# Performance work log

Hardware: AMD Instinct MI355X
Metric: run time of the kernel (lower is better)

The kernel has to match this reference:

```python
import jax, jax.numpy as jnp
import numpy as np

D_MODEL = 1024
NUM_HEADS = 16
HEAD_DIM = D_MODEL // NUM_HEADS


def setup_inputs() -> dict:
    key = jax.random.key(0)
    k0, k1, k2, k3, k4 = jax.random.split(key, 5)
    B, S, D = 4, 2048, D_MODEL
    std = np.sqrt(2.0 / (D + D)).astype(np.float32)
    return {
        "in_features": jax.random.normal(k0, (B, S, D), dtype=jnp.float32),
        "Wq": jax.random.normal(k1, (D, D), dtype=jnp.float32) * std,
        "Wk": jax.random.normal(k2, (D, D), dtype=jnp.float32) * std,
        "Wv": jax.random.normal(k3, (D, D), dtype=jnp.float32) * std,
        "Wo": jax.random.normal(k4, (D, D), dtype=jnp.float32) * std,
    }


def reference(in_features, Wq, Wk, Wv, Wo):
    B, S, D = in_features.shape
    H, Hd = NUM_HEADS, HEAD_DIM

    def split_heads(x):  # (B,S,D) -> (B,H,S,Hd)
        return x.reshape(B, S, H, Hd).transpose(0, 2, 1, 3)

    q = split_heads(in_features @ Wq.T)
    k = split_heads(in_features @ Wk.T)
    v = split_heads(in_features @ Wv.T)

    scale = 1.0 / jnp.sqrt(jnp.asarray(Hd, dtype=q.dtype))
    scores = jnp.einsum("bhsd,bhtd->bhst", q, k) * scale  # (B,H,S,S)
    causal = jnp.tril(jnp.ones((S, S), dtype=bool))  # (S,S)
    scores = jnp.where(causal[None, None], scores, -jnp.inf)
    attn = jax.nn.softmax(scores, axis=-1)
    out = jnp.einsum("bhst,bhtd->bhsd", attn, v)  # (B,H,S,Hd)
    out = out.transpose(0, 2, 1, 3).reshape(B, S, D)
    return out @ Wo.T
```

## Files before the change

kernel.cpp:

```cpp
#include <hip/hip_runtime.h>


typedef float f32x4 __attribute__((ext_vector_type(4)));
typedef float f32x16 __attribute__((ext_vector_type(16)));
typedef short s16x8 __attribute__((ext_vector_type(8)));

#if __has_builtin(__builtin_amdgcn_exp2f)
#define EXP2(x) __builtin_amdgcn_exp2f(x)
#else
#define EXP2(x) exp2f(x)
#endif

__device__ __forceinline__ unsigned short f2bf(float f) {
  unsigned int u = __float_as_uint(f);
  u += 0x7fffu + ((u >> 16) & 1u);
  return (unsigned short)(u >> 16);
}

__device__ __forceinline__ unsigned int pk2bf(float f0, float f1) {
  return __builtin_amdgcn_perm(__float_as_uint(f1) + 0x8000u,
                               __float_as_uint(f0) + 0x8000u, 0x07060302u);
}

__device__ __forceinline__ unsigned int pk2bf_t(float f0, float f1) {
  return __builtin_amdgcn_perm(__float_as_uint(f1), __float_as_uint(f0), 0x07060302u);
}

__device__ __forceinline__ void gl_lds16(const short* g, short* lds) {
  __builtin_amdgcn_global_load_lds(
      (const __attribute__((address_space(1))) unsigned int*)g,
      (__attribute__((address_space(3))) unsigned int*)lds, 16, 0, 0);
}

__global__ __launch_bounds__(256) void cvt_all(const float4* __restrict__ X,
                                               const float4* __restrict__ Wq,
                                               const float4* __restrict__ Wk,
                                               const float4* __restrict__ Wv,
                                               const float4* __restrict__ Wo,
                                               ushort4* __restrict__ xb,
                                               ushort4* __restrict__ wqkv,
                                               ushort4* __restrict__ wob) {
  const int NX = 8192 * 1024 / 4;
  const int NW = 1024 * 1024 / 4;
  const int NT = NX + 4 * NW;
  int i = blockIdx.x * blockDim.x + threadIdx.x;
  int stride = gridDim.x * blockDim.x;
  for (int idx = i; idx < NT; idx += stride) {
    const float4* s;
    ushort4* d;
    int off;
    if (idx < NX) {
      s = X; d = xb; off = idx;
    } else {
      int j = idx - NX;
      int w = j >> 18;
      off = j & (NW - 1);
      switch (w) {
        case 0: s = Wq; d = wqkv; break;
        case 1: s = Wk; d = wqkv + NW; break;
        case 2: s = Wv; d = wqkv + 2 * NW; break;
        default: s = Wo; d = wob; break;
      }
    }
    float4 f = s[off];
    ushort4 r;
    r.x = f2bf(f.x); r.y = f2bf(f.y); r.z = f2bf(f.z); r.w = f2bf(f.w);
    d[off] = r;
  }
}

template <int MODE>
__global__ __launch_bounds__(256) void gemm_bt(const short* __restrict__ A,
                                               const short* __restrict__ B,
                                               float* __restrict__ Cf,
                                               short* __restrict__ q_o,
                                               short* __restrict__ k_o,
                                               short* __restrict__ vT_o,
                                               int M, int N, int K) {
  const int tid = threadIdx.x;
  const int wave = tid >> 6, lane = tid & 63;
  const int quad = lane >> 4, l15 = lane & 15;
  const int m0 = blockIdx.x * 128, n0 = blockIdx.y * 128;
  const int wm = (wave >> 1) * 64, wn = (wave & 1) * 64;

  __shared__ __align__(16) short As[128 * 64];
  __shared__ __align__(16) short Bs[128 * 64];

  const f32x4 z4 = {0.f, 0.f, 0.f, 0.f};
  f32x4 acc[4][4];
  for (int i = 0; i < 4; ++i)
    for (int j = 0; j < 4; ++j) acc[i][j] = z4;

  for (int k0 = 0; k0 < K; k0 += 64) {
    __syncthreads();
    for (int i = 0; i < 4; ++i) {
      int c = wave * 4 + i;
      int r = c * 8 + (lane >> 3);
      int c8 = (lane & 7) ^ (r & 7);
      gl_lds16(A + (size_t)(m0 + r) * K + k0 + c8 * 8, As + c * 512 + lane * 8);
      gl_lds16(B + (size_t)(n0 + r) * K + k0 + c8 * 8, Bs + c * 512 + lane * 8);
    }
    __syncthreads();
    for (int kk = 0; kk < 64; kk += 32) {
      int c8b = (kk >> 3) + quad;
      s16x8 af[4], bfr[4];
      for (int mt = 0; mt < 4; ++mt) {
        int row = wm + mt * 16 + l15;
        af[mt] = *(const s16x8*)(As + row * 64 + ((c8b ^ (row & 7)) << 3));
      }
      for (int nt = 0; nt < 4; ++nt) {
        int row = wn + nt * 16 + l15;
        bfr[nt] = *(const s16x8*)(Bs + row * 64 + ((c8b ^ (row & 7)) << 3));
      }
      for (int mt = 0; mt < 4; ++mt)
        for (int nt = 0; nt < 4; ++nt)
          acc[mt][nt] = __builtin_amdgcn_mfma_f32_16x16x32_bf16(af[mt], bfr[nt],
                                                                acc[mt][nt], 0, 0, 0);
    }
  }

  if (MODE == 0) {
    for (int mt = 0; mt < 4; ++mt)
      for (int nt = 0; nt < 4; ++nt) {
        int col = n0 + wn + nt * 16 + l15;
        for (int r = 0; r < 4; ++r) {
          int row = m0 + wm + mt * 16 + quad * 4 + r;
          Cf[(size_t)row * N + col] = acc[mt][nt][r];
        }
      }
  } else {
    if (n0 < 1024) {
      const float scale = 0.18033688011112042f;
      for (int mt = 0; mt < 4; ++mt)
        for (int nt = 0; nt < 4; ++nt) {
          int col = n0 + wn + nt * 16 + l15;
          for (int r = 0; r < 4; ++r) {
            int row = m0 + wm + mt * 16 + quad * 4 + r;
            ((unsigned short*)q_o)[(size_t)row * 1024 + col] = f2bf(acc[mt][nt][r] * scale);
          }
        }
    } else if (n0 < 2048) {
      for (int mt = 0; mt < 4; ++mt)
        for (int nt = 0; nt < 4; ++nt) {
          int col = n0 - 1024 + wn + nt * 16 + l15;
          for (int r = 0; r < 4; ++r) {
            int row = m0 + wm + mt * 16 + quad * 4 + r;
            ((unsigned short*)k_o)[(size_t)row * 1024 + col] = f2bf(acc[mt][nt][r]);
          }
        }
    } else {
      for (int mt = 0; mt < 4; ++mt)
        for (int nt = 0; nt < 4; ++nt) {
          int col = n0 - 2048 + wn + nt * 16 + l15;
          int h = col >> 6, d = col & 63;
          int row0 = m0 + wm + mt * 16 + quad * 4;
          int b = row0 >> 11, s = row0 & 2047;
          uint2 pk;
          pk.x = pk2bf(acc[mt][nt][0], acc[mt][nt][1]);
          pk.y = pk2bf(acc[mt][nt][2], acc[mt][nt][3]);
          *(uint2*)((unsigned short*)vT_o + (((size_t)b * 16 + h) * 64 + d) * 2048 + s) = pk;
        }
    }
  }
}

__global__ __launch_bounds__(256, 2) void attn_kernel(const short* __restrict__ qb,
                                                      const short* __restrict__ kb,
                                                      const short* __restrict__ vT,
                                                      short* __restrict__ ob) {
  const int bh = blockIdx.x;
  const int qt = 15 - (int)blockIdx.y;
  const int tid = threadIdx.x;
  const int wave = tid >> 6, lane = tid & 63;
  const int l31 = lane & 31, h = lane >> 5;
  const int q0 = qt * 128;
  const size_t rowbase = (size_t)(bh >> 4) * 2048;
  const int hoff = (bh & 15) * 64;

  __shared__ __align__(16) short Ks[2][8192];
  __shared__ __align__(16) short VTs[2][8192];

  const int kc = wave * 4;
  const int kr = kc * 8 + (lane >> 3);
  const short* ksrc = kb + (rowbase + kr) * 1024 + hoff + (((lane & 7) ^ (kr & 7)) << 3);
  const int vg = lane & 15;
  const short* vsrc_i[4];
#pragma unroll
  for (int i = 0; i < 4; ++i) {
    int d = (kc + i) * 4 + (lane >> 4);
    vsrc_i[i] = vT + ((size_t)bh * 64 + d) * 2048 + ((vg ^ (d & 7)) << 3);
  }

  s16x8 qf[4];
  {
    const short* qrow = qb + (rowbase + q0 + wave * 32 + l31) * 1024 + hoff + h * 8;
#pragma unroll
    for (int k = 0; k < 4; ++k) qf[k] = *(const s16x8*)(qrow + k * 16);
  }

#pragma unroll
  for (int i = 0; i < 4; ++i)
    gl_lds16(ksrc + i * 8 * 1024, Ks[0] + (kc + i) * 512 + lane * 8);
#pragma unroll
  for (int i = 0; i < 4; ++i)
    gl_lds16(vsrc_i[i], VTs[0] + (kc + i) * 512 + lane * 8);

  f32x16 oacc[2];
#pragma unroll
  for (int dt = 0; dt < 2; ++dt)
#pragma unroll
    for (int e = 0; e < 16; ++e) oacc[dt][e] = 0.f;
  float lacc = 0.f;
  const int kswz = l31 & 7;

  for (int t = 0; t <= qt; ++t) {
    __syncthreads();
    const int cur = t & 1;

    if (t < qt) {
      const int nxt = cur ^ 1;
      const short* ks = ksrc + (size_t)(t + 1) * 128 * 1024;
#pragma unroll
      for (int i = 0; i < 4; ++i)
        gl_lds16(ks + i * 8 * 1024, Ks[nxt] + (kc + i) * 512 + lane * 8);
#pragma unroll
      for (int i = 0; i < 4; ++i)
        gl_lds16(vsrc_i[i] + (t + 1) * 128, VTs[nxt] + (kc + i) * 512 + lane * 8);
    }

    const short* Kc = Ks[cur];
    const short* Vc = VTs[cur];

    unsigned int pp[4][8];
    float sum = 0.f;
#pragma unroll
    for (int g = 0; g < 2; ++g) {
      f32x16 s0, s1;
#pragma unroll
      for (int e = 0; e < 16; ++e) { s0[e] = 0.f; s1[e] = 0.f; }
#pragma unroll
      for (int ks = 0; ks < 4; ++ks) {
        int pos = ((ks << 1) + h) ^ kswz;
        s16x8 kf0 = *(const s16x8*)(Kc + ((2 * g) * 32 + l31) * 64 + (pos << 3));
        s16x8 kf1 = *(const s16x8*)(Kc + ((2 * g + 1) * 32 + l31) * 64 + (pos << 3));
        s0 = __builtin_amdgcn_mfma_f32_32x32x16_bf16(kf0, qf[ks], s0, 0, 0, 0);
        s1 = __builtin_amdgcn_mfma_f32_32x32x16_bf16(kf1, qf[ks], s1, 0, 0, 0);
      }
      if (t == qt) {
        int qg = wave * 32 + l31;
#pragma unroll
        for (int e = 0; e < 16; ++e) {
          int rloc = (e & 3) + 8 * (e >> 2) + 4 * h;
          if ((2 * g) * 32 + rloc > qg) s0[e] = -1e30f;
          if ((2 * g + 1) * 32 + rloc > qg) s1[e] = -1e30f;
        }
      }
#pragma unroll
      for (int rg = 0; rg < 8; ++rg) {
        float a0 = EXP2(s0[2 * rg]), a1 = EXP2(s0[2 * rg + 1]);
        float b0 = EXP2(s1[2 * rg]), b1 = EXP2(s1[2 * rg + 1]);
        sum += (a0 + a1) + (b0 + b1);
        pp[2 * g][rg] = pk2bf_t(a0, a1);
        pp[2 * g + 1][rg] = pk2bf_t(b0, b1);
      }
    }
    lacc += sum;

#pragma unroll
    for (int s = 0; s < 8; ++s) {
      int m = s >> 1, base = (s & 1) * 4;
      unsigned int ax = pp[m][base + 0], ay = pp[m][base + 1];
      unsigned int bx = pp[m][base + 2], by = pp[m][base + 3];
      unsigned int sx = h ? ax : bx, sy = h ? ay : by;
      unsigned int rx = (unsigned int)__shfl_xor((int)sx, 32);
      unsigned int ry = (unsigned int)__shfl_xor((int)sy, 32);
      union { s16x8 v; unsigned int u[4]; } pf;
      pf.u[0] = h ? rx : ax;
      pf.u[1] = h ? ry : ay;
      pf.u[2] = h ? bx : rx;
      pf.u[3] = h ? by : ry;
#pragma unroll
      for (int dt = 0; dt < 2; ++dt) {
        int d = dt * 32 + l31;
        s16x8 vf = *(const s16x8*)(Vc + d * 128 + ((((s << 1) + h) ^ (d & 7)) << 3));
        oacc[dt] = __builtin_amdgcn_mfma_f32_32x32x16_bf16(vf, pf.v, oacc[dt], 0, 0, 0);
      }
    }
  }

  lacc += __shfl_xor(lacc, 32);
  float inv = 1.0f / lacc;
  size_t row = rowbase + q0 + wave * 32 + l31;
  unsigned short* orow = (unsigned short*)ob + row * 1024 + hoff;
#pragma unroll
  for (int dt = 0; dt < 2; ++dt)
#pragma unroll
    for (int rg = 0; rg < 4; ++rg) {
      int d = dt * 32 + rg * 8 + 4 * h;
      uint2 pk;
      pk.x = pk2bf(oacc[dt][rg * 4 + 0] * inv, oacc[dt][rg * 4 + 1] * inv);
      pk.y = pk2bf(oacc[dt][rg * 4 + 2] * inv, oacc[dt][rg * 4 + 3] * inv);
      *(uint2*)(orow + d) = pk;
    }
}

extern "C" void kernel_launch(void* const* d_in, const int* in_sizes, int n_in,
                              void* d_out, int out_size, void* d_ws, size_t ws_size,
                              hipStream_t stream) {
  const float* X  = (const float*)d_in[0];
  const float* Wq = (const float*)d_in[1];
  const float* Wk = (const float*)d_in[2];
  const float* Wv = (const float*)d_in[3];
  const float* Wo = (const float*)d_in[4];

  short* xb   = (short*)d_ws;
  short* wqkv = xb + (size_t)8192 * 1024;
  short* wob  = wqkv + (size_t)3072 * 1024;
  short* qb   = wob + (size_t)1024 * 1024;
  short* kb   = qb + (size_t)8192 * 1024;
  short* vT   = kb + (size_t)8192 * 1024;
  short* ob   = xb;

  const int MB = 8192;

  cvt_all<<<3072, 256, 0, stream>>>((const float4*)X, (const float4*)Wq, (const float4*)Wk,
                                    (const float4*)Wv, (const float4*)Wo, (ushort4*)xb,
                                    (ushort4*)wqkv, (ushort4*)wob);

  gemm_bt<1><<<dim3(64, 24), 256, 0, stream>>>(xb, wqkv, nullptr, qb, kb, vT, MB, 3072, 1024);

  attn_kernel<<<dim3(64, 16), 256, 0, stream>>>(qb, kb, vT, ob);

  gemm_bt<0><<<dim3(64, 8), 256, 0, stream>>>(ob, wob, (float*)d_out, nullptr, nullptr,
                                              nullptr, MB, 1024, 1024);
}
```

Before: 242.3 us.

## Single-buffer attention K/V staging for occupancy; double-buffer output-projection GEMM

The attention kernel drops its double-buffered K and V tiles for single buffers, which halves shared memory, and raises the launch bound to 4 blocks per CU. Within each tile it now loads V for the current tile before computing QK^T, and prefetches the next K after a mid-iteration barrier. This trades intra-block load/compute overlap for more resident blocks per CU, at the cost of one extra barrier per tile. Separately, the output-projection GEMM gets a double-buffered LDS prefetch path, so the next K-slice loads while the current one is multiplied. The QKV GEMM keeps the old single-buffer path.

```diff
diff --git a/kernel.cpp b/kernel.cpp
--- a/kernel.cpp
+++ b/kernel.cpp
@@ -69,7 +69,7 @@
   }
 }
 
-template <int MODE>
+template <int MODE, int DBUF>
 __global__ __launch_bounds__(256) void gemm_bt(const short* __restrict__ A,
                                                const short* __restrict__ B,
                                                float* __restrict__ Cf,
@@ -83,34 +83,63 @@
   const int m0 = blockIdx.x * 128, n0 = blockIdx.y * 128;
   const int wm = (wave >> 1) * 64, wn = (wave & 1) * 64;
 
-  __shared__ __align__(16) short As[128 * 64];
-  __shared__ __align__(16) short Bs[128 * 64];
+  __shared__ __align__(16) short As[(DBUF ? 2 : 1) * 8192];
+  __shared__ __align__(16) short Bs[(DBUF ? 2 : 1) * 8192];
 
   const f32x4 z4 = {0.f, 0.f, 0.f, 0.f};
   f32x4 acc[4][4];
   for (int i = 0; i < 4; ++i)
     for (int j = 0; j < 4; ++j) acc[i][j] = z4;
 
+  const int c0 = wave * 4;
+  const int r0 = c0 * 8 + (lane >> 3);
+  const int cc8 = lane & 7;
+
+  if (DBUF) {
+    for (int i = 0; i < 4; ++i) {
+      int r = r0 + i * 8;
+      int c8 = cc8 ^ (r & 7);
+      gl_lds16(A + (size_t)(m0 + r) * K + c8 * 8, As + (c0 + i) * 512 + lane * 8);
+      gl_lds16(B + (size_t)(n0 + r) * K + c8 * 8, Bs + (c0 + i) * 512 + lane * 8);
+    }
+  }
+
   for (int k0 = 0; k0 < K; k0 += 64) {
     __syncthreads();
-    for (int i = 0; i < 4; ++i) {
-      int c = wave * 4 + i;
-      int r = c * 8 + (lane >> 3);
-      int c8 = (lane & 7) ^ (r & 7);
-      gl_lds16(A + (size_t)(m0 + r) * K + k0 + c8 * 8, As + c * 512 + lane * 8);
-      gl_lds16(B + (size_t)(n0 + r) * K + k0 + c8 * 8, Bs + c * 512 + lane * 8);
-    }
-    __syncthreads();
+    const int cur = DBUF ? ((k0 >> 6) & 1) : 0;
+    if (DBUF) {
+      if (k0 + 64 < K) {
+        const int nxt = cur ^ 1;
+        for (int i = 0; i < 4; ++i) {
+          int r = r0 + i * 8;
+          int c8 = cc8 ^ (r & 7);
+          gl_lds16(A + (size_t)(m0 + r) * K + k0 + 64 + c8 * 8,
+                   As + nxt * 8192 + (c0 + i) * 512 + lane * 8);
+          gl_lds16(B + (size_t)(n0 + r) * K + k0 + 64 + c8 * 8,
+                   Bs + nxt * 8192 + (c0 + i) * 512 + lane * 8);
+        }
+      }
+    } else {
+      for (int i = 0; i < 4; ++i) {
+        int r = r0 + i * 8;
+        int c8 = cc8 ^ (r & 7);
+        gl_lds16(A + (size_t)(m0 + r) * K + k0 + c8 * 8, As + (c0 + i) * 512 + lane * 8);
+        gl_lds16(B + (size_t)(n0 + r) * K + k0 + c8 * 8, Bs + (c0 + i) * 512 + lane * 8);
+      }
+      __syncthreads();
+    }
+    const short* Ac = As + cur * 8192;
+    const short* Bc = Bs + cur * 8192;
     for (int kk = 0; kk < 64; kk += 32) {
       int c8b = (kk >> 3) + quad;
       s16x8 af[4], bfr[4];
       for (int mt = 0; mt < 4; ++mt) {
         int row = wm + mt * 16 + l15;
-        af[mt] = *(const s16x8*)(As + row * 64 + ((c8b ^ (row & 7)) << 3));
+        af[mt] = *(const s16x8*)(Ac + row * 64 + ((c8b ^ (row & 7)) << 3));
       }
       for (int nt = 0; nt < 4; ++nt) {
         int row = wn + nt * 16 + l15;
-        bfr[nt] = *(const s16x8*)(Bs + row * 64 + ((c8b ^ (row & 7)) << 3));
+        bfr[nt] = *(const s16x8*)(Bc + row * 64 + ((c8b ^ (row & 7)) << 3));
       }
       for (int mt = 0; mt < 4; ++mt)
         for (int nt = 0; nt < 4; ++nt)
@@ -164,7 +193,7 @@
   }
 }
 
-__global__ __launch_bounds__(256, 2) void attn_kernel(const short* __restrict__ qb,
+__global__ __launch_bounds__(256, 4) void attn_kernel(const short* __restrict__ qb,
                                                       const short* __restrict__ kb,
                                                       const short* __restrict__ vT,
                                                       short* __restrict__ ob) {
@@ -177,8 +206,8 @@
   const size_t rowbase = (size_t)(bh >> 4) * 2048;
   const int hoff = (bh & 15) * 64;
 
-  __shared__ __align__(16) short Ks[2][8192];
-  __shared__ __align__(16) short VTs[2][8192];
+  __shared__ __align__(16) short Ks[8192];
+  __shared__ __align__(16) short VTs[8192];
 
   const int kc = wave * 4;
   const int kr = kc * 8 + (lane >> 3);
@@ -200,10 +229,7 @@
 
 #pragma unroll
   for (int i = 0; i < 4; ++i)
-    gl_lds16(ksrc + i * 8 * 1024, Ks[0] + (kc + i) * 512 + lane * 8);
-#pragma unroll
-  for (int i = 0; i < 4; ++i)
-    gl_lds16(vsrc_i[i], VTs[0] + (kc + i) * 512 + lane * 8);
+    gl_lds16(ksrc + i * 8 * 1024, Ks + (kc + i) * 512 + lane * 8);
 
   f32x16 oacc[2];
 #pragma unroll
@@ -215,21 +241,10 @@
 
   for (int t = 0; t <= qt; ++t) {
     __syncthreads();
-    const int cur = t & 1;
-
-    if (t < qt) {
-      const int nxt = cur ^ 1;
-      const short* ks = ksrc + (size_t)(t + 1) * 128 * 1024;
-#pragma unroll
-      for (int i = 0; i < 4; ++i)
-        gl_lds16(ks + i * 8 * 1024, Ks[nxt] + (kc + i) * 512 + lane * 8);
-#pragma unroll
-      for (int i = 0; i < 4; ++i)
-        gl_lds16(vsrc_i[i] + (t + 1) * 128, VTs[nxt] + (kc + i) * 512 + lane * 8);
-    }
-
-    const short* Kc = Ks[cur];
-    const short* Vc = VTs[cur];
+
+#pragma unroll
+    for (int i = 0; i < 4; ++i)
+      gl_lds16(vsrc_i[i] + t * 128, VTs + (kc + i) * 512 + lane * 8);
 
     unsigned int pp[4][8];
     float sum = 0.f;
@@ -241,8 +256,8 @@
 #pragma unroll
       for (int ks = 0; ks < 4; ++ks) {
         int pos = ((ks << 1) + h) ^ kswz;
-        s16x8 kf0 = *(const s16x8*)(Kc + ((2 * g) * 32 + l31) * 64 + (pos << 3));
-        s16x8 kf1 = *(const s16x8*)(Kc + ((2 * g + 1) * 32 + l31) * 64 + (pos << 3));
+        s16x8 kf0 = *(const s16x8*)(Ks + ((2 * g) * 32 + l31) * 64 + (pos << 3));
+        s16x8 kf1 = *(const s16x8*)(Ks + ((2 * g + 1) * 32 + l31) * 64 + (pos << 3));
         s0 = __builtin_amdgcn_mfma_f32_32x32x16_bf16(kf0, qf[ks], s0, 0, 0, 0);
         s1 = __builtin_amdgcn_mfma_f32_32x32x16_bf16(kf1, qf[ks], s1, 0, 0, 0);
       }
@@ -265,6 +280,15 @@
       }
     }
     lacc += sum;
+
+    __syncthreads();
+
+    if (t < qt) {
+      const short* ks = ksrc + (size_t)(t + 1) * 128 * 1024;
+#pragma unroll
+      for (int i = 0; i < 4; ++i)
+        gl_lds16(ks + i * 8 * 1024, Ks + (kc + i) * 512 + lane * 8);
+    }
 
 #pragma unroll
     for (int s = 0; s < 8; ++s) {
@@ -282,7 +306,7 @@
 #pragma unroll
       for (int dt = 0; dt < 2; ++dt) {
         int d = dt * 32 + l31;
-        s16x8 vf = *(const s16x8*)(Vc + d * 128 + ((((s << 1) + h) ^ (d & 7)) << 3));
+        s16x8 vf = *(const s16x8*)(VTs + d * 128 + ((((s << 1) + h) ^ (d & 7)) << 3));
         oacc[dt] = __builtin_amdgcn_mfma_f32_32x32x16_bf16(vf, pf.v, oacc[dt], 0, 0, 0);
       }
     }
@@ -327,10 +351,11 @@
                                     (const float4*)Wv, (const float4*)Wo, (ushort4*)xb,
                                     (ushort4*)wqkv, (ushort4*)wob);
 
-  gemm_bt<1><<<dim3(64, 24), 256, 0, stream>>>(xb, wqkv, nullptr, qb, kb, vT, MB, 3072, 1024);
+  gemm_bt<1, 0><<<dim3(64, 24), 256, 0, stream>>>(xb, wqkv, nullptr, qb, kb, vT,
+                                                  MB, 3072, 1024);
 
   attn_kernel<<<dim3(64, 16), 256, 0, stream>>>(qb, kb, vT, ob);
 
-  gemm_bt<0><<<dim3(64, 8), 256, 0, stream>>>(ob, wob, (float*)d_out, nullptr, nullptr,
-                                              nullptr, MB, 1024, 1024);
-}
+  gemm_bt<0, 1><<<dim3(64, 8), 256, 0, stream>>>(ob, wob, (float*)d_out, nullptr, nullptr,
+                                                 nullptr, MB, 1024, 1024);
+}
```

Result: slower. 283.3 us (+16.9%).
